# Performance work log

Hardware: AMD Instinct MI355X
Metric: run time of the kernel (lower is better)

Reference implementation:

```python
import jax, jax.numpy as jnp
import numpy as np

B = 32768        # batch size
F_IN = 64        # numCommonFeatures
HID = 32         # numEmotionFeatures (and BatchNorm1d width)
E = 25           # emotionLength
G = 12           # numBasicEmotions
H = 8            # numInterpreterHeads
BN_EPS = 1e-5
L1_EPS = 1e-12   # F.normalize eps


def setup_inputs() -> dict:
    key = jax.random.key(0)
    ks = jax.random.split(key, 9)
    s1 = 1.0 / np.sqrt(F_IN)
    s2 = 1.0 / np.sqrt(HID)
    return {
        "inputData": jax.random.normal(ks[0], (B, F_IN), jnp.float32),
        # extractEmotionFeatures: Linear(64,32) -> SELU -> Linear(32,32) -> BN(32) -> SELU
        "W1": jax.random.uniform(ks[1], (F_IN, HID), jnp.float32, -s1, s1),
        "b1": jax.random.uniform(ks[2], (HID,), jnp.float32, -s1, s1),
        "W2": jax.random.uniform(ks[3], (HID, HID), jnp.float32, -s2, s2),
        "b2": jax.random.uniform(ks[4], (HID,), jnp.float32, -s2, s2),
        "gamma": jnp.ones((HID,), jnp.float32),
        "beta": jnp.zeros((HID,), jnp.float32),
        # 96 per-head Linear(32,25) stacked as one tensor [H, G, 32, 25]
        "Wh": jax.random.uniform(ks[5], (H, G, HID, E), jnp.float32, -s2, s2),
        "bh": jax.random.uniform(ks[6], (H, G, E), jnp.float32, -s2, s2),
    }


def reference(inputData, W1, b1, W2, b2, gamma, beta, Wh, bh):
    # shared feature extractor
    h = jax.nn.selu(inputData @ W1 + b1)          # [B, 32]
    h2 = h @ W2 + b2                               # [B, 32]
    # BatchNorm1d in training mode: biased batch statistics
    mu = h2.mean(axis=0)
    var = h2.var(axis=0)
    e = jax.nn.selu((h2 - mu) / jnp.sqrt(var + BN_EPS) * gamma + beta)  # [B, 32]
    # all 96 heads as one batched GEMM: [B,32] x [H,G,32,25] -> [B,H,G,25]
    d = jax.nn.selu(jnp.einsum('bf,hgfe->bhge', e, Wh) + bh)
    # sign * L1-normalize(|d|) along emotion axis (torch F.normalize p=1)
    a = jnp.abs(d)
    l1 = jnp.maximum(a.sum(axis=-1, keepdims=True), L1_EPS)
    return jnp.sign(d) * (a / l1)                  # [B, H, G, E]
```

## Files before the change

### kernel.cpp

```cpp
#include <hip/hip_runtime.h>
#include <stdint.h>

#define BATCH   32768
#define F_IN    64
#define HID     32
#define E_LEN   25
#define N_HG    96
#define BN_EPS  1e-5f

#define NBLK1   256

#define WS_WA   0
#define WS_BH   196608
#define WS_P1   212992
#define WS_P2   245760
#define WS_SS   278528
#define WS_H2   278784

typedef _Float16 half2_t __attribute__((ext_vector_type(2)));
typedef _Float16 f16x8   __attribute__((ext_vector_type(8)));
typedef float    f32x4   __attribute__((ext_vector_type(4)));

__device__ __forceinline__ float selu_f(float x) {
    const float lam = 1.0507009873554805f;
    const float la  = 1.7580993408473766f;
    return x > 0.f ? lam * x : la * (__expf(x) - 1.f);
}

__device__ __forceinline__ void compute_h2(const float* __restrict__ xr,
                                           const float* __restrict__ W1,
                                           const float* __restrict__ b1,
                                           const float* __restrict__ W2,
                                           const float* __restrict__ b2,
                                           float h2[HID]) {
    float x[F_IN];
    const float4* x4 = (const float4*)xr;
#pragma unroll
    for (int i = 0; i < F_IN / 4; ++i) {
        float4 v = x4[i];
        x[4*i] = v.x; x[4*i+1] = v.y; x[4*i+2] = v.z; x[4*i+3] = v.w;
    }
    float h[HID];
#pragma unroll
    for (int j = 0; j < HID; ++j) h[j] = b1[j];
#pragma unroll 4
    for (int i = 0; i < F_IN; ++i) {
        float xi = x[i];
#pragma unroll
        for (int j = 0; j < HID; ++j) h[j] = fmaf(xi, W1[i*HID + j], h[j]);
    }
#pragma unroll
    for (int j = 0; j < HID; ++j) h[j] = selu_f(h[j]);
#pragma unroll
    for (int j = 0; j < HID; ++j) h2[j] = b2[j];
#pragma unroll 4
    for (int k = 0; k < HID; ++k) {
        float hk = h[k];
#pragma unroll
        for (int j = 0; j < HID; ++j) h2[j] = fmaf(hk, W2[k*HID + j], h2[j]);
    }
}

__global__ __launch_bounds__(256) void k0_pack(const float* __restrict__ Wh,
                                               const float* __restrict__ bh,
                                               uint32_t* __restrict__ wA,
                                               float* __restrict__ bhp) {
    int t = blockIdx.x * 256 + threadIdx.x;
    if (t < N_HG * 2 * 64 * 4) {
        int q    = t & 3;
        int lane = (t >> 2) & 63;
        int tl   = (t >> 8) & 1;
        int hg   = t >> 9;
        int ee   = (lane & 15) + 16 * tl;
        int g    = lane >> 4;
        int f0   = g * 8 + q * 2;
        float a = 0.f, b = 0.f;
        if (ee < E_LEN) {
            a = Wh[hg * (HID * E_LEN) + f0 * E_LEN + ee];
            b = Wh[hg * (HID * E_LEN) + (f0 + 1) * E_LEN + ee];
        }
        half2_t p; p[0] = (_Float16)a; p[1] = (_Float16)b;
        wA[t] = __builtin_bit_cast(uint32_t, p);
    } else {
        int id = t - N_HG * 2 * 64 * 4;
        if (id < N_HG * HID) {
            int hg = id >> 5, ee = id & 31;
            bhp[id] = (ee < E_LEN) ? bh[hg * E_LEN + ee] : 0.f;
        }
    }
}

__global__ __launch_bounds__(128) void k1_stats(const float* __restrict__ inp,
                                               const float* __restrict__ W1,
                                               const float* __restrict__ b1,
                                               const float* __restrict__ W2,
                                               const float* __restrict__ b2,
                                               float* __restrict__ h2out,
                                               float* __restrict__ p1,
                                               float* __restrict__ p2) {
    int tid  = threadIdx.x;
    int row  = blockIdx.x * 128 + tid;
    int lane = tid & 63;
    int wv   = tid >> 6;

    float h2[HID];
    compute_h2(inp + (size_t)row * F_IN, W1, b1, W2, b2, h2);

    float4* dst = (float4*)(h2out + (size_t)row * HID);
#pragma unroll
    for (int k = 0; k < HID / 4; ++k)
        dst[k] = make_float4(h2[4*k], h2[4*k+1], h2[4*k+2], h2[4*k+3]);

    __shared__ float s1[2][HID];
    __shared__ float s2[2][HID];
#pragma unroll
    for (int j = 0; j < HID; ++j) {
        float a = h2[j];
        float b = h2[j] * h2[j];
#pragma unroll
        for (int off = 32; off > 0; off >>= 1) {
            a += __shfl_xor(a, off, 64);
            b += __shfl_xor(b, off, 64);
        }
        if (lane == 0) { s1[wv][j] = a; s2[wv][j] = b; }
    }
    __syncthreads();
    if (tid < HID) {
        p1[blockIdx.x * HID + tid] = s1[0][tid] + s1[1][tid];
        p2[blockIdx.x * HID + tid] = s2[0][tid] + s2[1][tid];
    }
}

__global__ __launch_bounds__(256) void k2_fold(const float* __restrict__ p1,
                                               const float* __restrict__ p2,
                                               const float* __restrict__ gamma,
                                               const float* __restrict__ beta,
                                               float* __restrict__ ss) {
    __shared__ float l1[8][HID];
    __shared__ float l2[8][HID];
    int f = threadIdx.x & 31;
    int c = threadIdx.x >> 5;
    float a = 0.f, b = 0.f;
    for (int i = c; i < NBLK1; i += 8) {
        a += p1[i * HID + f];
        b += p2[i * HID + f];
    }
    l1[c][f] = a; l2[c][f] = b;
    __syncthreads();
    if (threadIdx.x < HID) {
        float A = 0.f, Bv = 0.f;
#pragma unroll
        for (int i = 0; i < 8; ++i) { A += l1[i][f]; Bv += l2[i][f]; }
        float mu  = A * (1.0f / (float)BATCH);
        float var = Bv * (1.0f / (float)BATCH) - mu * mu;
        float sc  = gamma[f] * rsqrtf(var + BN_EPS);
        ss[f]        = sc;
        ss[HID + f]  = beta[f] - mu * sc;
    }
}

#define K4_GPB 24
#define K4_GS  28
#define K4_STR 676

__global__ __launch_bounds__(256, 3) void k4_heads(const float* __restrict__ h2buf,
                                                   const float* __restrict__ ss,
                                                   const uint32_t* __restrict__ wA,
                                                   const float* __restrict__ bhp,
                                                   float* __restrict__ out) {
    __shared__ float tile[16 * K4_STR];

    int tid  = threadIdx.x;
    int lane = tid & 63;
    int wave = __builtin_amdgcn_readfirstlane(tid >> 6);
    int q    = blockIdx.x & 3;
    int r0   = (blockIdx.x >> 2) * 16;
    int grp  = lane >> 4;
    int col  = lane & 15;

    uint4 aw[6][2];
#pragma unroll
    for (int c = 0; c < 6; ++c) {
        int hg = q * K4_GPB + wave * 6 + c;
#pragma unroll
        for (int t = 0; t < 2; ++t)
            aw[c][t] = *(const uint4*)(wA + ((hg * 2 + t) * 64 + lane) * 4);
    }

    f16x8 Bf;
    {
        const float* hrow = h2buf + (size_t)(r0 + col) * HID + grp * 8;
        float4 h0  = *(const float4*)hrow;
        float4 h1  = *(const float4*)(hrow + 4);
        float4 sc0 = *(const float4*)(ss + grp * 8);
        float4 sc1 = *(const float4*)(ss + grp * 8 + 4);
        float4 sh0 = *(const float4*)(ss + HID + grp * 8);
        float4 sh1 = *(const float4*)(ss + HID + grp * 8 + 4);
        float e0 = selu_f(fmaf(h0.x, sc0.x, sh0.x));
        float e1 = selu_f(fmaf(h0.y, sc0.y, sh0.y));
        float e2 = selu_f(fmaf(h0.z, sc0.z, sh0.z));
        float e3 = selu_f(fmaf(h0.w, sc0.w, sh0.w));
        float e4 = selu_f(fmaf(h1.x, sc1.x, sh1.x));
        float e5 = selu_f(fmaf(h1.y, sc1.y, sh1.y));
        float e6 = selu_f(fmaf(h1.z, sc1.z, sh1.z));
        float e7 = selu_f(fmaf(h1.w, sc1.w, sh1.w));
        f16x8 b;
        b[0] = (_Float16)e0; b[1] = (_Float16)e1; b[2] = (_Float16)e2; b[3] = (_Float16)e3;
        b[4] = (_Float16)e4; b[5] = (_Float16)e5; b[6] = (_Float16)e6; b[7] = (_Float16)e7;
        Bf = b;
    }

#pragma unroll
    for (int c = 0; c < 6; ++c) {
        int hg = q * K4_GPB + wave * 6 + c;
        int gl = wave * 6 + c;
        f32x4 zero = {0.f, 0.f, 0.f, 0.f};
        f32x4 d0 = __builtin_amdgcn_mfma_f32_16x16x32_f16(
                       __builtin_bit_cast(f16x8, aw[c][0]), Bf, zero, 0, 0, 0);
        f32x4 d1 = __builtin_amdgcn_mfma_f32_16x16x32_f16(
                       __builtin_bit_cast(f16x8, aw[c][1]), Bf, zero, 0, 0, 0);
        float4 b0 = *(const float4*)(bhp + hg * HID + grp * 4);
        float4 b1 = *(const float4*)(bhp + hg * HID + 16 + grp * 4);

        float v0[4], v1[4];
        float l1 = 0.f;
        {
            float bb[4] = {b0.x, b0.y, b0.z, b0.w};
#pragma unroll
            for (int r = 0; r < 4; ++r) {
                float x = selu_f(d0[r] + bb[r]);
                v0[r] = x; l1 += fabsf(x);
            }
        }
        {
            float bb[4] = {b1.x, b1.y, b1.z, b1.w};
#pragma unroll
            for (int r = 0; r < 4; ++r) {
                int ee1 = 16 + grp * 4 + r;
                float x = (ee1 < E_LEN) ? selu_f(d1[r] + bb[r]) : 0.f;
                v1[r] = x; l1 += fabsf(x);
            }
        }
        l1 += __shfl_xor(l1, 16, 64);
        l1 += __shfl_xor(l1, 32, 64);
        float inv = 1.0f / fmaxf(l1, 1e-12f);

        float* tb = &tile[col * K4_STR + gl * K4_GS];
        *(float4*)(tb + grp * 4) =
            make_float4(v0[0] * inv, v0[1] * inv, v0[2] * inv, v0[3] * inv);
        if (grp < 3)
            *(float4*)(tb + 16 + grp * 4) =
                make_float4(v1[0] * inv, v1[1] * inv, v1[2] * inv, v1[3] * inv);
    }
    asm volatile("s_waitcnt lgkmcnt(0)" ::: "memory");
    __builtin_amdgcn_s_barrier();

    float* ob = out + (size_t)r0 * (N_HG * E_LEN) + q * (K4_GPB * E_LEN);
    for (int i4 = tid; i4 < 16 * 150; i4 += 256) {
        int rr = i4 / 150;
        unsigned w = (unsigned)(i4 - rr * 150) * 4u;
        const float* trow = &tile[rr * K4_STR];
        float4 v;
        v.x = trow[w     + 3u * ((w     ) / 25u)];
        v.y = trow[w + 1u + 3u * ((w + 1u) / 25u)];
        v.z = trow[w + 2u + 3u * ((w + 2u) / 25u)];
        v.w = trow[w + 3u + 3u * ((w + 3u) / 25u)];
        *(float4*)(ob + (size_t)rr * (N_HG * E_LEN) + w) = v;
    }
}

extern "C" void kernel_launch(void* const* d_in, const int* in_sizes, int n_in,
                              void* d_out, int out_size, void* d_ws, size_t ws_size,
                              hipStream_t stream) {
    const float* inp   = (const float*)d_in[0];
    const float* W1    = (const float*)d_in[1];
    const float* b1    = (const float*)d_in[2];
    const float* W2    = (const float*)d_in[3];
    const float* b2    = (const float*)d_in[4];
    const float* gamma = (const float*)d_in[5];
    const float* beta  = (const float*)d_in[6];
    const float* Wh    = (const float*)d_in[7];
    const float* bh    = (const float*)d_in[8];
    float* out = (float*)d_out;

    char* ws = (char*)d_ws;
    uint32_t* wAb = (uint32_t*)(ws + WS_WA);
    float*    bhp = (float*)(ws + WS_BH);
    float*    p1  = (float*)(ws + WS_P1);
    float*    p2  = (float*)(ws + WS_P2);
    float*    ssb = (float*)(ws + WS_SS);
    float*    h2b = (float*)(ws + WS_H2);

    hipLaunchKernelGGL(k0_pack,  dim3(204),   dim3(256), 0, stream, Wh, bh, wAb, bhp);
    hipLaunchKernelGGL(k1_stats, dim3(NBLK1), dim3(128), 0, stream, inp, W1, b1, W2, b2, h2b, p1, p2);
    hipLaunchKernelGGL(k2_fold,  dim3(1),     dim3(256), 0, stream, p1, p2, gamma, beta, ssb);
    hipLaunchKernelGGL(k4_heads, dim3((BATCH / 16) * 4), dim3(256), 0, stream, h2b, ssb, wAb, bhp, out);
}
```

Baseline: 421.6 us.

## Fuse weight packing with stats kernel and compute MLP via split-fp16 MFMA

Merges the head-weight packing kernel and the feature-extractor/statistics kernel into one launch. The packing blocks come first, followed by 512 blocks that compute both small linear layers with MFMA instructions. The MFMA path uses a hi/lo fp16 split with three products to approximate fp32 accuracy, replacing per-thread scalar FMA loops. This removes one launch and the heavy scalar ALU work per row. The trade-off is some loss of precision from dropping the lo*lo term, plus twice as many partial sums for the fold kernel to reduce.

```diff
diff --git a/kernel.cpp b/kernel.cpp
--- a/kernel.cpp
+++ b/kernel.cpp
@@ -8,16 +8,18 @@
 #define N_HG    96
 #define BN_EPS  1e-5f
 
-#define NBLK1   256
+#define PACKB   193
+#define NBLK1   512
 
 #define WS_WA   0
 #define WS_BH   196608
 #define WS_P1   212992
-#define WS_P2   245760
-#define WS_SS   278528
-#define WS_H2   278784
+#define WS_P2   278528
+#define WS_SS   344064
+#define WS_H2   344320
 
 typedef _Float16 half2_t __attribute__((ext_vector_type(2)));
+typedef _Float16 f16x4   __attribute__((ext_vector_type(4)));
 typedef _Float16 f16x8   __attribute__((ext_vector_type(8)));
 typedef float    f32x4   __attribute__((ext_vector_type(4)));
 
@@ -27,46 +29,28 @@
     return x > 0.f ? lam * x : la * (__expf(x) - 1.f);
 }
 
-__device__ __forceinline__ void compute_h2(const float* __restrict__ xr,
-                                           const float* __restrict__ W1,
-                                           const float* __restrict__ b1,
-                                           const float* __restrict__ W2,
-                                           const float* __restrict__ b2,
-                                           float h2[HID]) {
-    float x[F_IN];
-    const float4* x4 = (const float4*)xr;
-#pragma unroll
-    for (int i = 0; i < F_IN / 4; ++i) {
-        float4 v = x4[i];
-        x[4*i] = v.x; x[4*i+1] = v.y; x[4*i+2] = v.z; x[4*i+3] = v.w;
-    }
-    float h[HID];
-#pragma unroll
-    for (int j = 0; j < HID; ++j) h[j] = b1[j];
-#pragma unroll 4
-    for (int i = 0; i < F_IN; ++i) {
-        float xi = x[i];
-#pragma unroll
-        for (int j = 0; j < HID; ++j) h[j] = fmaf(xi, W1[i*HID + j], h[j]);
-    }
-#pragma unroll
-    for (int j = 0; j < HID; ++j) h[j] = selu_f(h[j]);
-#pragma unroll
-    for (int j = 0; j < HID; ++j) h2[j] = b2[j];
-#pragma unroll 4
-    for (int k = 0; k < HID; ++k) {
-        float hk = h[k];
-#pragma unroll
-        for (int j = 0; j < HID; ++j) h2[j] = fmaf(hk, W2[k*HID + j], h2[j]);
-    }
-}
-
-__global__ __launch_bounds__(256) void k0_pack(const float* __restrict__ Wh,
-                                               const float* __restrict__ bh,
-                                               uint32_t* __restrict__ wA,
-                                               float* __restrict__ bhp) {
-    int t = blockIdx.x * 256 + threadIdx.x;
-    if (t < N_HG * 2 * 64 * 4) {
+__device__ __forceinline__ uint32_t pk2(float a, float b) {
+    half2_t p; p[0] = (_Float16)a; p[1] = (_Float16)b;
+    return __builtin_bit_cast(uint32_t, p);
+}
+
+__global__ __launch_bounds__(256) void k01_fused(const float* __restrict__ inp,
+                                                 const float* __restrict__ W1,
+                                                 const float* __restrict__ b1,
+                                                 const float* __restrict__ W2,
+                                                 const float* __restrict__ b2,
+                                                 const float* __restrict__ Wh,
+                                                 const float* __restrict__ bh,
+                                                 uint32_t* __restrict__ wA,
+                                                 float* __restrict__ bhp,
+                                                 float* __restrict__ h2out,
+                                                 float* __restrict__ p1,
+                                                 float* __restrict__ p2) {
+    int tid = threadIdx.x;
+    int bid = blockIdx.x;
+
+    if (bid < 192) {
+        int t    = bid * 256 + tid;
         int q    = t & 3;
         int lane = (t >> 2) & 63;
         int tl   = (t >> 8) & 1;
@@ -79,55 +63,152 @@
             a = Wh[hg * (HID * E_LEN) + f0 * E_LEN + ee];
             b = Wh[hg * (HID * E_LEN) + (f0 + 1) * E_LEN + ee];
         }
-        half2_t p; p[0] = (_Float16)a; p[1] = (_Float16)b;
-        wA[t] = __builtin_bit_cast(uint32_t, p);
-    } else {
-        int id = t - N_HG * 2 * 64 * 4;
-        if (id < N_HG * HID) {
-            int hg = id >> 5, ee = id & 31;
-            bhp[id] = (ee < E_LEN) ? bh[hg * E_LEN + ee] : 0.f;
-        }
-    }
-}
-
-__global__ __launch_bounds__(128) void k1_stats(const float* __restrict__ inp,
-                                               const float* __restrict__ W1,
-                                               const float* __restrict__ b1,
-                                               const float* __restrict__ W2,
-                                               const float* __restrict__ b2,
-                                               float* __restrict__ h2out,
-                                               float* __restrict__ p1,
-                                               float* __restrict__ p2) {
-    int tid  = threadIdx.x;
-    int row  = blockIdx.x * 128 + tid;
+        wA[t] = pk2(a, b);
+        return;
+    }
+    if (bid < PACKB) {
+        for (int i = tid; i < N_HG * HID; i += 256) {
+            int hg = i >> 5, ee = i & 31;
+            bhp[i] = (ee < E_LEN) ? bh[hg * E_LEN + ee] : 0.f;
+        }
+        return;
+    }
+
+    __shared__ float sP1[4][HID];
+    __shared__ float sP2[4][HID];
+
+    int sb   = bid - PACKB;
     int lane = tid & 63;
     int wv   = tid >> 6;
-
-    float h2[HID];
-    compute_h2(inp + (size_t)row * F_IN, W1, b1, W2, b2, h2);
-
-    float4* dst = (float4*)(h2out + (size_t)row * HID);
-#pragma unroll
-    for (int k = 0; k < HID / 4; ++k)
-        dst[k] = make_float4(h2[4*k], h2[4*k+1], h2[4*k+2], h2[4*k+3]);
-
-    __shared__ float s1[2][HID];
-    __shared__ float s2[2][HID];
-#pragma unroll
-    for (int j = 0; j < HID; ++j) {
-        float a = h2[j];
-        float b = h2[j] * h2[j];
-#pragma unroll
-        for (int off = 32; off > 0; off >>= 1) {
-            a += __shfl_xor(a, off, 64);
-            b += __shfl_xor(b, off, 64);
-        }
-        if (lane == 0) { s1[wv][j] = a; s2[wv][j] = b; }
+    int c    = lane & 15;
+    int q    = lane >> 4;
+    int r0   = (sb * 4 + wv) * 16;
+
+    f16x8 W1hf[2][2], W1lf[2][2];
+#pragma unroll
+    for (int t = 0; t < 2; ++t)
+#pragma unroll
+        for (int s = 0; s < 2; ++s) {
+            f16x8 hi, lo;
+#pragma unroll
+            for (int j = 0; j < 8; ++j) {
+                float v = W1[(32 * s + 8 * q + j) * HID + 16 * t + c];
+                _Float16 hv = (_Float16)v;
+                hi[j] = hv;
+                lo[j] = (_Float16)(v - (float)hv);
+            }
+            W1hf[t][s] = hi; W1lf[t][s] = lo;
+        }
+    f16x4 W2hf[2][2], W2lf[2][2];
+#pragma unroll
+    for (int t = 0; t < 2; ++t)
+#pragma unroll
+        for (int s = 0; s < 2; ++s) {
+            f16x4 hi, lo;
+#pragma unroll
+            for (int j = 0; j < 4; ++j) {
+                float v = W2[(16 * s + 4 * q + j) * HID + 16 * t + c];
+                _Float16 hv = (_Float16)v;
+                hi[j] = hv;
+                lo[j] = (_Float16)(v - (float)hv);
+            }
+            W2hf[t][s] = hi; W2lf[t][s] = lo;
+        }
+
+    f16x8 Bh[2], Bl[2];
+    {
+        const float* xr = inp + (size_t)(r0 + c) * F_IN;
+#pragma unroll
+        for (int s = 0; s < 2; ++s) {
+            float4 a = *(const float4*)(xr + 32 * s + 8 * q);
+            float4 b = *(const float4*)(xr + 32 * s + 8 * q + 4);
+            float e[8] = {a.x, a.y, a.z, a.w, b.x, b.y, b.z, b.w};
+            f16x8 hi, lo;
+#pragma unroll
+            for (int j = 0; j < 8; ++j) {
+                _Float16 h = (_Float16)e[j];
+                hi[j] = h;
+                lo[j] = (_Float16)(e[j] - (float)h);
+            }
+            Bh[s] = hi; Bl[s] = lo;
+        }
+    }
+
+    f32x4 D[2];
+#pragma unroll
+    for (int t = 0; t < 2; ++t) {
+        f32x4 acc = {0.f, 0.f, 0.f, 0.f};
+#pragma unroll
+        for (int s = 0; s < 2; ++s) {
+            acc = __builtin_amdgcn_mfma_f32_16x16x32_f16(W1hf[t][s], Bh[s], acc, 0, 0, 0);
+            acc = __builtin_amdgcn_mfma_f32_16x16x32_f16(W1lf[t][s], Bh[s], acc, 0, 0, 0);
+            acc = __builtin_amdgcn_mfma_f32_16x16x32_f16(W1hf[t][s], Bl[s], acc, 0, 0, 0);
+        }
+        D[t] = acc;
+    }
+
+    f16x4 Hh[2], Hl[2];
+#pragma unroll
+    for (int t = 0; t < 2; ++t) {
+        float4 bv = *(const float4*)(b1 + 16 * t + 4 * q);
+        float bb[4] = {bv.x, bv.y, bv.z, bv.w};
+        f16x4 hi, lo;
+#pragma unroll
+        for (int r = 0; r < 4; ++r) {
+            float h = selu_f(D[t][r] + bb[r]);
+            _Float16 hh = (_Float16)h;
+            hi[r] = hh;
+            lo[r] = (_Float16)(h - (float)hh);
+        }
+        Hh[t] = hi; Hl[t] = lo;
+    }
+
+    float h2v[2][4];
+#pragma unroll
+    for (int t = 0; t < 2; ++t) {
+        f32x4 acc = {0.f, 0.f, 0.f, 0.f};
+#pragma unroll
+        for (int s = 0; s < 2; ++s) {
+            acc = __builtin_amdgcn_mfma_f32_16x16x16f16(W2hf[t][s], Hh[s], acc, 0, 0, 0);
+            acc = __builtin_amdgcn_mfma_f32_16x16x16f16(W2lf[t][s], Hh[s], acc, 0, 0, 0);
+            acc = __builtin_amdgcn_mfma_f32_16x16x16f16(W2hf[t][s], Hl[s], acc, 0, 0, 0);
+        }
+        float4 bv = *(const float4*)(b2 + 16 * t + 4 * q);
+        float bb[4] = {bv.x, bv.y, bv.z, bv.w};
+#pragma unroll
+        for (int r = 0; r < 4; ++r) h2v[t][r] = acc[r] + bb[r];
+    }
+
+#pragma unroll
+    for (int t = 0; t < 2; ++t)
+        *(float4*)(h2out + (size_t)(r0 + c) * HID + 16 * t + 4 * q) =
+            make_float4(h2v[t][0], h2v[t][1], h2v[t][2], h2v[t][3]);
+
+#pragma unroll
+    for (int t = 0; t < 2; ++t) {
+#pragma unroll
+        for (int r = 0; r < 4; ++r) {
+            float a = h2v[t][r];
+            float b = a * a;
+#pragma unroll
+            for (int off = 1; off < 16; off <<= 1) {
+                a += __shfl_xor(a, off, 64);
+                b += __shfl_xor(b, off, 64);
+            }
+            if (c == 0) {
+                int j2 = 16 * t + 4 * q + r;
+                sP1[wv][j2] = a;
+                sP2[wv][j2] = b;
+            }
+        }
     }
     __syncthreads();
     if (tid < HID) {
-        p1[blockIdx.x * HID + tid] = s1[0][tid] + s1[1][tid];
-        p2[blockIdx.x * HID + tid] = s2[0][tid] + s2[1][tid];
+        float A = 0.f, B = 0.f;
+#pragma unroll
+        for (int w = 0; w < 4; ++w) { A += sP1[w][tid]; B += sP2[w][tid]; }
+        p1[sb * HID + tid] = A;
+        p2[sb * HID + tid] = B;
     }
 }
 
@@ -291,8 +372,9 @@
     float*    ssb = (float*)(ws + WS_SS);
     float*    h2b = (float*)(ws + WS_H2);
 
-    hipLaunchKernelGGL(k0_pack,  dim3(204),   dim3(256), 0, stream, Wh, bh, wAb, bhp);
-    hipLaunchKernelGGL(k1_stats, dim3(NBLK1), dim3(128), 0, stream, inp, W1, b1, W2, b2, h2b, p1, p2);
-    hipLaunchKernelGGL(k2_fold,  dim3(1),     dim3(256), 0, stream, p1, p2, gamma, beta, ssb);
+    hipLaunchKernelGGL(k01_fused, dim3(PACKB + NBLK1), dim3(256), 0, stream,
+                       inp, W1, b1, W2, b2, Wh, bh,
+                       wAb, bhp, h2b, p1, p2);
+    hipLaunchKernelGGL(k2_fold,  dim3(1),    dim3(256), 0, stream, p1, p2, gamma, beta, ssb);
     hipLaunchKernelGGL(k4_heads, dim3((BATCH / 16) * 4), dim3(256), 0, stream, h2b, ssb, wAb, bhp, out);
 }
```

Result: faster. 395.5 us (-6.2%).
